# Kernel tuning notes

Hardware: AMD Instinct MI355X
Metric: run time of the kernel (lower is better)

Reference implementation:

```python
import jax, jax.numpy as jnp
import numpy as np

A_VOCAB = 400000   # embedding table rows (a)
D = 200            # embedding_dim, hard-coded as 200 in the original module
C = 50000          # number of concepts
T = 1000000        # total flattened ancestor entries (~20 per concept)
B = 1024           # batch of input vectors x


def setup_inputs() -> dict:
    key = jax.random.key(0)
    k1, k2, k3, k4 = jax.random.split(key, 4)
    return {
        "x": jax.random.normal(k1, (B, D), dtype=jnp.float32),
        "embed_weight": jax.random.normal(k2, (A_VOCAB, D), dtype=jnp.float32) * 0.02,
        "ancestor_ids": jax.random.randint(k3, (T,), 0, A_VOCAB, dtype=jnp.int32),
        "segment_ids": jnp.sort(jax.random.randint(k4, (T,), 0, C, dtype=jnp.int32)),
        "n_concepts": C,
    }


def reference(x, embed_weight, ancestor_ids, segment_ids, n_concepts):
    # Ragged gather + per-concept sum (the original's Python loop over concepts)
    gathered = embed_weight[ancestor_ids]                                   # [T, D]
    local_H = jax.ops.segment_sum(gathered, segment_ids,
                                  num_segments=n_concepts)                  # [C, D]
    # concept_vector = local_H @ x.T ; output = softmax(concept_vector.T, dim=1)
    logits = jnp.einsum('bd,cd->bc', x, local_H)                            # [B, C]
    return jax.nn.softmax(logits, axis=1)
```

## Files before the change

### kernel.cpp

```cpp
#include <hip/hip_runtime.h>
#include <hip/hip_bf16.h>

#define DDIM   200
#define CSEG   50000
#define TTOT   1000000
#define BROWS  1024
#define KPAD   224
#define NTILE  64
#define NT     782
#define NPAD   50048
#define MTILES 8
#define GEMM_BLOCKS (NT * MTILES)
#define LDSROW 232

typedef __attribute__((ext_vector_type(8))) __bf16 bf16x8;
typedef __attribute__((ext_vector_type(4))) float  f32x4;
typedef unsigned short u16;
typedef __attribute__((ext_vector_type(8))) unsigned short u16x8;
typedef __attribute__((ext_vector_type(4))) unsigned short u16x4;

#define WS_XB    0u
#define WS_HB    458752u
#define WS_PART  (WS_HB + 22421504u)
#define WS_INV   (WS_PART + 3203072u)
#define WS_START (WS_INV + 4096u)
#define WS_EBF   (WS_START + 200704u)
#define WS_TOTAL_BF16 ((size_t)WS_EBF + 160000000u)

__device__ inline u16 f2bf(float f) {
  unsigned u = __float_as_uint(f);
  u += 0x7FFFu + ((u >> 16) & 1u);
  return (u16)(u >> 16);
}
__device__ inline float bf2f(u16 h) {
  return __uint_as_float(((unsigned)h) << 16);
}

__global__ __launch_bounds__(256) void fused_prep_kernel(const int* __restrict__ sid,
                                                         int* __restrict__ start,
                                                         const float* __restrict__ x,
                                                         u16* __restrict__ xb) {
  const int gtid = blockIdx.x * 256 + threadIdx.x;
  if (gtid < TTOT) {
    const int cur = sid[gtid];
    const int prev = (gtid == 0) ? -1 : sid[gtid - 1];
    for (int c = prev + 1; c <= cur; ++c) start[c] = gtid;
    if (gtid == TTOT - 1) {
      for (int c = cur + 1; c <= CSEG; ++c) start[c] = TTOT;
    }
  }
  if (gtid < BROWS * 56) {
    const int row = gtid / 56;
    const int col = (gtid % 56) * 4;
    ushort4 o = make_ushort4(0, 0, 0, 0);
    if (col < DDIM) {
      const float4 v = *reinterpret_cast<const float4*>(x + (size_t)row * DDIM + col);
      o = make_ushort4(f2bf(v.x), f2bf(v.y), f2bf(v.z), f2bf(v.w));
    }
    *reinterpret_cast<ushort4*>(xb + (size_t)row * KPAD + col) = o;
  }
}

__global__ __launch_bounds__(256) void conv_embed_kernel(const float* __restrict__ embed,
                                                         u16* __restrict__ ebf) {
  const long long n4 = (long long)400000 * DDIM / 4;
  const long long stride = (long long)gridDim.x * 256;
  for (long long i = (long long)blockIdx.x * 256 + threadIdx.x; i < n4; i += stride) {
    const f32x4 v = __builtin_nontemporal_load(reinterpret_cast<const f32x4*>(embed) + i);
    u16x4 o;
    o.x = f2bf(v.x); o.y = f2bf(v.y); o.z = f2bf(v.z); o.w = f2bf(v.w);
    *(reinterpret_cast<u16x4*>(ebf) + i) = o;
  }
}

__global__ __launch_bounds__(256) void seg_sum_bf16_kernel(const u16* __restrict__ ebf,
                                                           const int* __restrict__ aid,
                                                           const int* __restrict__ start,
                                                           u16* __restrict__ Hb) {
  const int wave = threadIdx.x >> 6;
  const int lane = threadIdx.x & 63;
  const int c = blockIdx.x * 4 + wave;
  if (c >= NPAD || lane >= 56) return;
  const int col = lane * 4;
  const bool act = (col < DDIM);
  float4 a[8];
#pragma unroll
  for (int j = 0; j < 8; ++j) a[j] = make_float4(0.f, 0.f, 0.f, 0.f);
  if (c < CSEG && act) {
    const int s = start[c], e = start[c + 1];
    for (int t = s; t < e; t += 8) {
      int   idx[8];
      float msk[8];
#pragma unroll
      for (int j = 0; j < 8; ++j) {
        const int tt = t + j;
        const bool ok = (tt < e);
        idx[j] = aid[ok ? tt : s];
        msk[j] = ok ? 1.f : 0.f;
      }
#pragma unroll
      for (int j = 0; j < 8; ++j) {
        const ushort4 v = *reinterpret_cast<const ushort4*>(
            ebf + (size_t)idx[j] * DDIM + col);
        a[j].x = fmaf(msk[j], bf2f(v.x), a[j].x);
        a[j].y = fmaf(msk[j], bf2f(v.y), a[j].y);
        a[j].z = fmaf(msk[j], bf2f(v.z), a[j].z);
        a[j].w = fmaf(msk[j], bf2f(v.w), a[j].w);
      }
    }
#pragma unroll
    for (int j = 4; j < 8; ++j) {
      a[j - 4].x += a[j].x; a[j - 4].y += a[j].y;
      a[j - 4].z += a[j].z; a[j - 4].w += a[j].w;
    }
    a[0].x += a[1].x + a[2].x + a[3].x;
    a[0].y += a[1].y + a[2].y + a[3].y;
    a[0].z += a[1].z + a[2].z + a[3].z;
    a[0].w += a[1].w + a[2].w + a[3].w;
  }
  const ushort4 o = (c < CSEG && act)
      ? make_ushort4(f2bf(a[0].x), f2bf(a[0].y), f2bf(a[0].z), f2bf(a[0].w))
      : make_ushort4(0, 0, 0, 0);
  *reinterpret_cast<ushort4*>(Hb + (size_t)c * KPAD + col) = o;
}

__global__ __launch_bounds__(256) void seg_sum_kernel(const float* __restrict__ embed,
                                                      const int* __restrict__ aid,
                                                      const int* __restrict__ start,
                                                      u16* __restrict__ Hb) {
  const int wave = threadIdx.x >> 6;
  const int lane = threadIdx.x & 63;
  const int c = blockIdx.x * 4 + wave;
  if (c >= NPAD || lane >= 56) return;
  const int col = lane * 4;
  const bool act = (col < DDIM);
  float4 a[8];
#pragma unroll
  for (int j = 0; j < 8; ++j) a[j] = make_float4(0.f, 0.f, 0.f, 0.f);
  if (c < CSEG && act) {
    const int s = start[c], e = start[c + 1];
    for (int t = s; t < e; t += 8) {
      int   idx[8];
      float msk[8];
#pragma unroll
      for (int j = 0; j < 8; ++j) {
        const int tt = t + j;
        const bool ok = (tt < e);
        idx[j] = aid[ok ? tt : s];
        msk[j] = ok ? 1.f : 0.f;
      }
#pragma unroll
      for (int j = 0; j < 8; ++j) {
        const float4 v = *reinterpret_cast<const float4*>(
            embed + (size_t)idx[j] * DDIM + col);
        a[j].x = fmaf(msk[j], v.x, a[j].x);
        a[j].y = fmaf(msk[j], v.y, a[j].y);
        a[j].z = fmaf(msk[j], v.z, a[j].z);
        a[j].w = fmaf(msk[j], v.w, a[j].w);
      }
    }
#pragma unroll
    for (int j = 4; j < 8; ++j) {
      a[j - 4].x += a[j].x; a[j - 4].y += a[j].y;
      a[j - 4].z += a[j].z; a[j - 4].w += a[j].w;
    }
    a[0].x += a[1].x + a[2].x + a[3].x;
    a[0].y += a[1].y + a[2].y + a[3].y;
    a[0].z += a[1].z + a[2].z + a[3].z;
    a[0].w += a[1].w + a[2].w + a[3].w;
  }
  const ushort4 o = (c < CSEG && act)
      ? make_ushort4(f2bf(a[0].x), f2bf(a[0].y), f2bf(a[0].z), f2bf(a[0].w))
      : make_ushort4(0, 0, 0, 0);
  *reinterpret_cast<ushort4*>(Hb + (size_t)c * KPAD + col) = o;
}

__device__ inline void gemm_block_map(int orig, int* ntile, int* mtile) {
  const int f = (orig & 7) * (GEMM_BLOCKS / 8) + (orig >> 3);
  *ntile = f >> 3;
  *mtile = f & 7;
}

__device__ inline void gemm_tile_lds(const u16* __restrict__ xb,
                                     const u16* __restrict__ Hb,
                                     u16* hlds, int m0, int n0, int tid,
                                     f32x4 acc[2][4]) {
  const int lane = tid & 63;
  const int r  = lane & 15;
  const int ko = (lane >> 4) * 8;
  const u16* xp = xb + (size_t)(m0 + r) * KPAD + ko;
  bf16x8 afrag[7][2];
#pragma unroll
  for (int ks = 0; ks < 7; ++ks) {
    afrag[ks][0] = *reinterpret_cast<const bf16x8*>(xp + ks * 32);
    afrag[ks][1] = *reinterpret_cast<const bf16x8*>(xp + 16 * KPAD + ks * 32);
  }
#pragma unroll
  for (int k = 0; k < 7; ++k) {
    const int i = tid + k * 256;
    const int row = i / 28, c8 = i % 28;
    const u16x8 h = *reinterpret_cast<const u16x8*>(
        Hb + (size_t)(n0 + row) * KPAD + c8 * 8);
    *reinterpret_cast<u16x8*>(hlds + row * LDSROW + c8 * 8) = h;
  }
  __syncthreads();
#pragma unroll
  for (int ks = 0; ks < 7; ++ks) {
#pragma unroll
    for (int ni = 0; ni < 4; ++ni) {
      const bf16x8 b = *reinterpret_cast<const bf16x8*>(
          hlds + (r + ni * 16) * LDSROW + ko + ks * 32);
      acc[0][ni] = __builtin_amdgcn_mfma_f32_16x16x32_bf16(afrag[ks][0], b, acc[0][ni], 0, 0, 0);
      acc[1][ni] = __builtin_amdgcn_mfma_f32_16x16x32_bf16(afrag[ks][1], b, acc[1][ni], 0, 0, 0);
    }
  }
}

__global__ __launch_bounds__(256) void gemm_pass1_kernel(const u16* __restrict__ xb,
                                                         const u16* __restrict__ Hb,
                                                         float* __restrict__ partials) {
  __shared__ u16 hlds[64 * LDSROW];
  int ntile, mtile;
  gemm_block_map(blockIdx.x, &ntile, &mtile);
  const int lane = threadIdx.x & 63, wave = threadIdx.x >> 6;
  const int m0 = mtile * 128 + wave * 32;
  const int n0 = ntile * NTILE;
  f32x4 acc[2][4] = {};
  gemm_tile_lds(xb, Hb, hlds, m0, n0, threadIdx.x, acc);
  const int cbase = n0 + (lane & 15);
#pragma unroll
  for (int mi = 0; mi < 2; ++mi) {
#pragma unroll
    for (int rr = 0; rr < 4; ++rr) {
      float s = 0.f;
#pragma unroll
      for (int ni = 0; ni < 4; ++ni) {
        if (cbase + ni * 16 < CSEG) s += __expf(acc[mi][ni][rr]);
      }
      for (int off = 1; off < 16; off <<= 1) s += __shfl_xor(s, off, 64);
      if ((lane & 15) == 0) {
        const int row = m0 + mi * 16 + (lane >> 4) * 4 + rr;
        partials[(size_t)row * NT + ntile] = s;
      }
    }
  }
}

__global__ __launch_bounds__(256) void reduce_kernel(const float* __restrict__ partials,
                                                     float* __restrict__ invs) {
  const int row = blockIdx.x, tid = threadIdx.x;
  float s = 0.f;
  for (int nt = tid; nt < NT; nt += 256) s += partials[(size_t)row * NT + nt];
  __shared__ float sm[256];
  sm[tid] = s;
  __syncthreads();
  for (int st = 128; st > 0; st >>= 1) {
    if (tid < st) sm[tid] += sm[tid + st];
    __syncthreads();
  }
  if (tid == 0) invs[row] = 1.0f / sm[0];
}

__global__ __launch_bounds__(256) void gemm_pass2_kernel(const u16* __restrict__ xb,
                                                         const u16* __restrict__ Hb,
                                                         const float* __restrict__ invs,
                                                         float* __restrict__ out) {
  __shared__ u16 hlds[64 * LDSROW];
  int ntile, mtile;
  gemm_block_map(blockIdx.x, &ntile, &mtile);
  const int lane = threadIdx.x & 63, wave = threadIdx.x >> 6;
  const int m0 = mtile * 128 + wave * 32;
  const int n0 = ntile * NTILE;
  f32x4 acc[2][4] = {};
  gemm_tile_lds(xb, Hb, hlds, m0, n0, threadIdx.x, acc);
  const int c0 = n0 + (lane & 15);
#pragma unroll
  for (int mi = 0; mi < 2; ++mi) {
#pragma unroll
    for (int rr = 0; rr < 4; ++rr) {
      const int row = m0 + mi * 16 + (lane >> 4) * 4 + rr;
      const float inv = invs[row];
      float* orow = out + (size_t)row * CSEG;
#pragma unroll
      for (int ni = 0; ni < 4; ++ni) {
        const int col = c0 + ni * 16;
        if (col < CSEG) {
          __builtin_nontemporal_store(__expf(acc[mi][ni][rr]) * inv, &orow[col]);
        }
      }
    }
  }
}

extern "C" void kernel_launch(void* const* d_in, const int* in_sizes, int n_in,
                              void* d_out, int out_size, void* d_ws, size_t ws_size,
                              hipStream_t stream) {
  const float* x     = (const float*)d_in[0];
  const float* embed = (const float*)d_in[1];
  const int*   aid   = (const int*)d_in[2];
  const int*   sid   = (const int*)d_in[3];

  char* ws = (char*)d_ws;
  u16*   xb       = (u16*)(ws + WS_XB);
  u16*   Hb       = (u16*)(ws + WS_HB);
  float* partials = (float*)(ws + WS_PART);
  float* invs     = (float*)(ws + WS_INV);
  int*   start    = (int*)(ws + WS_START);
  u16*   ebf      = (u16*)(ws + WS_EBF);
  float* out      = (float*)d_out;

  const bool use_bf16 = (ws_size >= WS_TOTAL_BF16);

  hipLaunchKernelGGL(fused_prep_kernel, dim3((TTOT + 255) / 256), dim3(256), 0, stream,
                     sid, start, x, xb);
  if (use_bf16) {
    hipLaunchKernelGGL(conv_embed_kernel, dim3(2048), dim3(256), 0, stream, embed, ebf);
    hipLaunchKernelGGL(seg_sum_bf16_kernel, dim3(NPAD / 4), dim3(256), 0, stream,
                       ebf, aid, start, Hb);
  } else {
    hipLaunchKernelGGL(seg_sum_kernel, dim3(NPAD / 4), dim3(256), 0, stream,
                       embed, aid, start, Hb);
  }
  hipLaunchKernelGGL(gemm_pass1_kernel, dim3(GEMM_BLOCKS), dim3(256), 0, stream,
                     xb, Hb, partials);
  hipLaunchKernelGGL(reduce_kernel,     dim3(BROWS),       dim3(256), 0, stream,
                     partials, invs);
  hipLaunchKernelGGL(gemm_pass2_kernel, dim3(GEMM_BLOCKS), dim3(256), 0, stream,
                     xb, Hb, invs, out);
}
```

Baseline: 273.3 us.

## Fuse embed bf16 conversion into prep kernel and widen seg-sum gathers

```diff
diff --git a/kernel.cpp b/kernel.cpp
--- a/kernel.cpp
+++ b/kernel.cpp
@@ -36,10 +36,13 @@
   return __uint_as_float(((unsigned)h) << 16);
 }
 
-__global__ __launch_bounds__(256) void fused_prep_kernel(const int* __restrict__ sid,
-                                                         int* __restrict__ start,
-                                                         const float* __restrict__ x,
-                                                         u16* __restrict__ xb) {
+__global__ __launch_bounds__(256) void prep_all_kernel(const int* __restrict__ sid,
+                                                       int* __restrict__ start,
+                                                       const float* __restrict__ x,
+                                                       u16* __restrict__ xb,
+                                                       const float* __restrict__ embed,
+                                                       u16* __restrict__ ebf,
+                                                       int do_conv) {
   const int gtid = blockIdx.x * 256 + threadIdx.x;
   if (gtid < TTOT) {
     const int cur = sid[gtid];
@@ -59,17 +62,15 @@
     }
     *reinterpret_cast<ushort4*>(xb + (size_t)row * KPAD + col) = o;
   }
-}
-
-__global__ __launch_bounds__(256) void conv_embed_kernel(const float* __restrict__ embed,
-                                                         u16* __restrict__ ebf) {
-  const long long n4 = (long long)400000 * DDIM / 4;
-  const long long stride = (long long)gridDim.x * 256;
-  for (long long i = (long long)blockIdx.x * 256 + threadIdx.x; i < n4; i += stride) {
-    const f32x4 v = __builtin_nontemporal_load(reinterpret_cast<const f32x4*>(embed) + i);
-    u16x4 o;
-    o.x = f2bf(v.x); o.y = f2bf(v.y); o.z = f2bf(v.z); o.w = f2bf(v.w);
-    *(reinterpret_cast<u16x4*>(ebf) + i) = o;
+  if (do_conv) {
+    const long long n4 = (long long)400000 * DDIM / 4;
+    const long long stride = (long long)gridDim.x * 256;
+    for (long long i = gtid; i < n4; i += stride) {
+      const f32x4 v = __builtin_nontemporal_load(reinterpret_cast<const f32x4*>(embed) + i);
+      u16x4 o;
+      o.x = f2bf(v.x); o.y = f2bf(v.y); o.z = f2bf(v.z); o.w = f2bf(v.w);
+      *(reinterpret_cast<u16x4*>(ebf) + i) = o;
+    }
   }
 }
 
@@ -80,48 +81,49 @@
   const int wave = threadIdx.x >> 6;
   const int lane = threadIdx.x & 63;
   const int c = blockIdx.x * 4 + wave;
-  if (c >= NPAD || lane >= 56) return;
-  const int col = lane * 4;
-  const bool act = (col < DDIM);
-  float4 a[8];
-#pragma unroll
-  for (int j = 0; j < 8; ++j) a[j] = make_float4(0.f, 0.f, 0.f, 0.f);
-  if (c < CSEG && act) {
+  if (c >= NPAD) return;
+  const int chunk = (lane < 50) ? (lane % 25) : 0;
+  const int par   = (lane < 50) ? (lane / 25) : 0;
+  float acc[8] = {0.f, 0.f, 0.f, 0.f, 0.f, 0.f, 0.f, 0.f};
+  if (c < CSEG && lane < 50) {
     const int s = start[c], e = start[c + 1];
-    for (int t = s; t < e; t += 8) {
+    for (int tb = s; tb < e; tb += 16) {
       int   idx[8];
       float msk[8];
 #pragma unroll
       for (int j = 0; j < 8; ++j) {
-        const int tt = t + j;
+        const int tt = tb + 2 * j + par;
         const bool ok = (tt < e);
         idx[j] = aid[ok ? tt : s];
         msk[j] = ok ? 1.f : 0.f;
       }
 #pragma unroll
       for (int j = 0; j < 8; ++j) {
-        const ushort4 v = *reinterpret_cast<const ushort4*>(
-            ebf + (size_t)idx[j] * DDIM + col);
-        a[j].x = fmaf(msk[j], bf2f(v.x), a[j].x);
-        a[j].y = fmaf(msk[j], bf2f(v.y), a[j].y);
-        a[j].z = fmaf(msk[j], bf2f(v.z), a[j].z);
-        a[j].w = fmaf(msk[j], bf2f(v.w), a[j].w);
-      }
-    }
-#pragma unroll
-    for (int j = 4; j < 8; ++j) {
-      a[j - 4].x += a[j].x; a[j - 4].y += a[j].y;
-      a[j - 4].z += a[j].z; a[j - 4].w += a[j].w;
-    }
-    a[0].x += a[1].x + a[2].x + a[3].x;
-    a[0].y += a[1].y + a[2].y + a[3].y;
-    a[0].z += a[1].z + a[2].z + a[3].z;
-    a[0].w += a[1].w + a[2].w + a[3].w;
-  }
-  const ushort4 o = (c < CSEG && act)
-      ? make_ushort4(f2bf(a[0].x), f2bf(a[0].y), f2bf(a[0].z), f2bf(a[0].w))
-      : make_ushort4(0, 0, 0, 0);
-  *reinterpret_cast<ushort4*>(Hb + (size_t)c * KPAD + col) = o;
+        const u16x8 v = *reinterpret_cast<const u16x8*>(
+            ebf + (size_t)idx[j] * DDIM + chunk * 8);
+#pragma unroll
+        for (int k = 0; k < 8; ++k) {
+          acc[k] = fmaf(msk[j], bf2f(v[k]), acc[k]);
+        }
+      }
+    }
+  }
+  const int src = (lane + 25) & 63;
+#pragma unroll
+  for (int k = 0; k < 8; ++k) {
+    acc[k] += __shfl(acc[k], src, 64);
+  }
+  if (lane < 28) {
+    u16x8 o;
+    if (lane < 25 && c < CSEG) {
+#pragma unroll
+      for (int k = 0; k < 8; ++k) o[k] = f2bf(acc[k]);
+    } else {
+#pragma unroll
+      for (int k = 0; k < 8; ++k) o[k] = 0;
+    }
+    *reinterpret_cast<u16x8*>(Hb + (size_t)c * KPAD + lane * 8) = o;
+  }
 }
 
 __global__ __launch_bounds__(256) void seg_sum_kernel(const float* __restrict__ embed,
@@ -311,10 +313,9 @@
 
   const bool use_bf16 = (ws_size >= WS_TOTAL_BF16);
 
-  hipLaunchKernelGGL(fused_prep_kernel, dim3((TTOT + 255) / 256), dim3(256), 0, stream,
-                     sid, start, x, xb);
+  hipLaunchKernelGGL(prep_all_kernel, dim3((TTOT + 255) / 256), dim3(256), 0, stream,
+                     sid, start, x, xb, embed, ebf, use_bf16 ? 1 : 0);
   if (use_bf16) {
-    hipLaunchKernelGGL(conv_embed_kernel, dim3(2048), dim3(256), 0, stream, embed, ebf);
     hipLaunchKernelGGL(seg_sum_bf16_kernel, dim3(NPAD / 4), dim3(256), 0, stream,
                        ebf, aid, start, Hb);
   } else {
```

Result: no change. 268.8 us (median of 2 runs) (-1.6%).
